# Kernel tuning notes

Hardware: AMD Instinct MI355X
Metric: run time of the kernel (lower is better)

The kernel has to match this reference:

```python
import jax, jax.numpy as jnp
import numpy as np

D_MODEL = 512
N_HEADS = 8
HEAD_DIM = D_MODEL // N_HEADS
D_FF = 2048
RADIUS = 1                      # manhattan_radius
MAX_LEVEL = 2                   # layer_max_level
WINDOWS = (512, 64, 16)         # window_size_per_level


def _layer_norm(x, g, b, eps=1e-5):
    mu = jnp.mean(x, axis=-1, keepdims=True)
    var = jnp.mean(jnp.square(x - mu), axis=-1, keepdims=True)
    return (x - mu) * jax.lax.rsqrt(var + eps) * g + b


def setup_inputs() -> dict:
    key = jax.random.key(0)
    ks = jax.random.split(key, 16)
    B, N = 2, 2048
    s = 0.02
    return {
        "x": jax.random.normal(ks[0], (B, N, D_MODEL), jnp.float32),
        "coords_pos": jax.random.randint(ks[1], (B, N, 2), 0, 64, jnp.int32),
        "coords_level": jax.random.randint(ks[2], (B, N), 0, 3, jnp.int32),
        "w_qkv": jax.random.normal(ks[3], (D_MODEL, 3 * D_MODEL), jnp.float32) * s,
        "b_qkv": jnp.zeros((3 * D_MODEL,), jnp.float32),
        "w_out": jax.random.normal(ks[4], (D_MODEL, D_MODEL), jnp.float32) * s,
        "b_out": jnp.zeros((D_MODEL,), jnp.float32),
        "w_ff1": jax.random.normal(ks[5], (D_MODEL, D_FF), jnp.float32) * s,
        "b_ff1": jnp.zeros((D_FF,), jnp.float32),
        "w_ff2": jax.random.normal(ks[6], (D_FF, D_MODEL), jnp.float32) * s,
        "b_ff2": jnp.zeros((D_MODEL,), jnp.float32),
        "ln1_g": jnp.ones((D_MODEL,), jnp.float32),
        "ln1_b": jnp.zeros((D_MODEL,), jnp.float32),
        "ln2_g": jnp.ones((D_MODEL,), jnp.float32),
        "ln2_b": jnp.zeros((D_MODEL,), jnp.float32),
    }


def _geometric_mask(coords_pos, coords_level):
    """[B,N,N] bool mask: same hierarchy level, Manhattan distance <= RADIUS,
    within the per-level sequence window, levels <= MAX_LEVEL; self always allowed."""
    B, N = coords_level.shape
    # Manhattan distance on grid coords  [B,N,N]
    dist = jnp.sum(jnp.abs(coords_pos[:, :, None, :] - coords_pos[:, None, :, :]), axis=-1)
    same_level = coords_level[:, :, None] == coords_level[:, None, :]
    lvl_ok = coords_level <= MAX_LEVEL                       # [B,N]
    lvl_pair = lvl_ok[:, :, None] & lvl_ok[:, None, :]
    win_tab = jnp.array(WINDOWS, jnp.int32)
    win_q = win_tab[jnp.clip(coords_level, 0, len(WINDOWS) - 1)]  # [B,N]
    idx = jnp.arange(N, dtype=jnp.int32)
    seq_dist = jnp.abs(idx[:, None] - idx[None, :])          # [N,N]
    in_window = seq_dist[None] < win_q[:, :, None]
    eye = jnp.eye(N, dtype=bool)[None]
    return (same_level & (dist <= RADIUS) & in_window & lvl_pair) | eye


def reference(x, coords_pos, coords_level, w_qkv, b_qkv, w_out, b_out,
              w_ff1, b_ff1, w_ff2, b_ff2, ln1_g, ln1_b, ln2_g, ln2_b):
    B, N, D = x.shape
    residual = x
    xn = _layer_norm(x, ln1_g, ln1_b)
    qkv = (xn @ w_qkv + b_qkv).reshape(B, N, 3, N_HEADS, HEAD_DIM)
    q, k, v = qkv[:, :, 0], qkv[:, :, 1], qkv[:, :, 2]        # [B,N,H,Dh]

    scale = 1.0 / np.sqrt(HEAD_DIM)
    scores = jnp.einsum("bihd,bjhd->bhij", q, k) * scale      # [B,H,N,N]
    mask = _geometric_mask(coords_pos, coords_level)          # [B,N,N]
    scores = jnp.where(mask[:, None], scores, jnp.float32(-1e9))
    probs = jax.nn.softmax(scores, axis=-1)
    attn = jnp.einsum("bhij,bjhd->bihd", probs, v).reshape(B, N, D)
    x = residual + (attn @ w_out + b_out)                     # dropout = identity (eval)

    residual = x
    xn = _layer_norm(x, ln2_g, ln2_b)
    h = jax.nn.gelu(xn @ w_ff1 + b_ff1, approximate=False)
    x = residual + (h @ w_ff2 + b_ff2)
    return x
```

## Files before the change

### kernel.cpp

```cpp
#include <hip/hip_runtime.h>
#include <hip/hip_bf16.h>

#define DMODEL 512
#define NHEADS 8
#define DFF 2048
#define NSEQ 2048
#define NROWS 4096

typedef __attribute__((ext_vector_type(8))) short   bf16x8;
typedef __attribute__((ext_vector_type(4))) float   f32x4;
typedef __attribute__((ext_vector_type(8))) unsigned short u16x8;

__device__ __forceinline__ unsigned short f2bf(float f) {
  union { float f; unsigned u; } v; v.f = f;
  unsigned r = v.u + 0x7fffu + ((v.u >> 16) & 1u);
  return (unsigned short)(r >> 16);
}
__device__ __forceinline__ float bf2f(unsigned short u) {
  union { unsigned u; float f; } v; v.u = (unsigned)u << 16;
  return v.f;
}

#define GLL16(src, dst) \
  __builtin_amdgcn_global_load_lds((__attribute__((address_space(1))) const void*)(src), \
                                   (__attribute__((address_space(3))) void*)(dst), 16, 0, 0)

__global__ __launch_bounds__(64)
void ln_kernel(const float* __restrict__ x, const float* __restrict__ g,
               const float* __restrict__ b, unsigned short* __restrict__ out) {
  const int row = blockIdx.x;
  const int lane = threadIdx.x;
  const float* xr = x + (size_t)row * DMODEL + lane * 8;
  const float4 v0 = *(const float4*)(xr);
  const float4 v1 = *(const float4*)(xr + 4);
  float s  = v0.x + v0.y + v0.z + v0.w + v1.x + v1.y + v1.z + v1.w;
  float s2 = v0.x*v0.x + v0.y*v0.y + v0.z*v0.z + v0.w*v0.w
           + v1.x*v1.x + v1.y*v1.y + v1.z*v1.z + v1.w*v1.w;
  #pragma unroll
  for (int m = 1; m < 64; m <<= 1) {
    s  += __shfl_xor(s,  m);
    s2 += __shfl_xor(s2, m);
  }
  const float mu  = s * (1.0f / DMODEL);
  const float var = s2 * (1.0f / DMODEL) - mu * mu;
  const float rs  = rsqrtf(var + 1e-5f);
  const float4 g0 = *(const float4*)(g + lane * 8);
  const float4 g1 = *(const float4*)(g + lane * 8 + 4);
  const float4 b0 = *(const float4*)(b + lane * 8);
  const float4 b1 = *(const float4*)(b + lane * 8 + 4);
  u16x8 o;
  o[0] = f2bf((v0.x - mu) * rs * g0.x + b0.x);
  o[1] = f2bf((v0.y - mu) * rs * g0.y + b0.y);
  o[2] = f2bf((v0.z - mu) * rs * g0.z + b0.z);
  o[3] = f2bf((v0.w - mu) * rs * g0.w + b0.w);
  o[4] = f2bf((v1.x - mu) * rs * g1.x + b1.x);
  o[5] = f2bf((v1.y - mu) * rs * g1.y + b1.y);
  o[6] = f2bf((v1.z - mu) * rs * g1.z + b1.z);
  o[7] = f2bf((v1.w - mu) * rs * g1.w + b1.w);
  *(u16x8*)(out + (size_t)row * DMODEL + lane * 8) = o;
}

__global__ __launch_bounds__(256)
void wt_all(const float* __restrict__ w0, unsigned short* __restrict__ t0,
            const float* __restrict__ w1, unsigned short* __restrict__ t1,
            const float* __restrict__ w2, unsigned short* __restrict__ t2,
            const float* __restrict__ w3, unsigned short* __restrict__ t3) {
  __shared__ unsigned short t[32][33];
  int bid = blockIdx.x;
  const float* w; unsigned short* wT; int K, N;
  if (bid < 768)       { w = w0; wT = t0; K = 512;  N = 1536; }
  else if (bid < 1024) { bid -= 768;  w = w1; wT = t1; K = 512;  N = 512; }
  else if (bid < 2048) { bid -= 1024; w = w2; wT = t2; K = 512;  N = 2048; }
  else                 { bid -= 2048; w = w3; wT = t3; K = 2048; N = 512; }
  const int ntx = N >> 5;
  const int n0 = (bid % ntx) * 32, k0 = (bid / ntx) * 32;
  const int tx = threadIdx.x, ty = threadIdx.y;
  #pragma unroll
  for (int i = 0; i < 4; ++i)
    t[ty + i * 8][tx] = f2bf(w[(size_t)(k0 + ty + i * 8) * N + n0 + tx]);
  __syncthreads();
  #pragma unroll
  for (int i = 0; i < 4; ++i)
    wT[(size_t)(n0 + ty + i * 8) * K + k0 + tx] = t[tx][ty + i * 8];
}

template<int MODE, int BM>
__global__ __launch_bounds__(256)
void gemm_bf16(const unsigned short* __restrict__ A,
               const unsigned short* __restrict__ Bt,
               const float* __restrict__ bias, const float* __restrict__ res,
               void* __restrict__ Cout, int M, int N, int LDA, int KL) {
  constexpr int MR = BM / 32;
  constexpr int PS = BM / 32 + 2;
  __shared__ unsigned short As[3][BM * 64];
  __shared__ unsigned short Bs[3][64 * 64];

  const int tid = threadIdx.x;
  const int w = tid >> 6, l = tid & 63;
  const int gx = N >> 6;
  const int nxy = gx * (M / BM);
  int lin = blockIdx.x;
  lin = (lin & 7) * (nxy >> 3) + (lin >> 3);
  const int bn = (lin % gx) << 6;
  const int bm = (lin / gx) * BM;
  const int wr = (w >> 1) * (BM >> 1);
  const int wc = (w & 1) * 32;
  const int lr = l & 15, kg = l >> 4;

  f32x4 acc[MR][2] = {};

  auto stage = [&](int buf, int k0) {
    #pragma unroll
    for (int i = 0; i < BM / 32; ++i) {
      const int g = i * 4 + w;
      const int c = g * 64 + l;
      const int row = c >> 3, kc = c & 7;
      GLL16(A + (size_t)(bm + row) * LDA + k0 + kc * 8, &As[buf][g * 512]);
    }
    #pragma unroll
    for (int i = 0; i < 2; ++i) {
      const int g = i * 4 + w;
      const int c = g * 64 + l;
      const int row = c >> 3, kc = c & 7;
      GLL16(Bt + (size_t)(bn + row) * LDA + k0 + kc * 8, &Bs[buf][g * 512]);
    }
  };

  const int nt = KL >> 6;
  stage(0, 0);
  stage(1, 64);
  for (int t = 0; t < nt; ++t) {
    if (t + 1 < nt) {
      asm volatile("s_waitcnt vmcnt(%0)" :: "n"(PS) : "memory");
    } else {
      asm volatile("s_waitcnt vmcnt(0)" ::: "memory");
    }
    __builtin_amdgcn_sched_barrier(0);
    __builtin_amdgcn_s_barrier();
    __builtin_amdgcn_sched_barrier(0);
    if (t + 2 < nt) stage((t + 2) % 3, (t + 2) << 6);
    const int cur = t % 3;
    #pragma unroll
    for (int ks = 0; ks < 2; ++ks) {
      const int cc = ks * 4 + kg;
      bf16x8 af[MR], bfv[2];
      #pragma unroll
      for (int mi = 0; mi < MR; ++mi)
        af[mi] = *(const bf16x8*)&As[cur][(wr + mi * 16 + lr) * 64 + cc * 8];
      #pragma unroll
      for (int ni = 0; ni < 2; ++ni)
        bfv[ni] = *(const bf16x8*)&Bs[cur][(wc + ni * 16 + lr) * 64 + cc * 8];
      __builtin_amdgcn_s_setprio(1);
      #pragma unroll
      for (int mi = 0; mi < MR; ++mi)
        #pragma unroll
        for (int ni = 0; ni < 2; ++ni)
          acc[mi][ni] = __builtin_amdgcn_mfma_f32_16x16x32_bf16(
              af[mi], bfv[ni], acc[mi][ni], 0, 0, 0);
      __builtin_amdgcn_s_setprio(0);
    }
  }

  float* Cf = (float*)Cout;
  unsigned short* Cb = (unsigned short*)Cout;
  #pragma unroll
  for (int mi = 0; mi < MR; ++mi) {
    #pragma unroll
    for (int ni = 0; ni < 2; ++ni) {
      const int gcol = bn + wc + ni * 16 + lr;
      const int grow0 = bm + wr + mi * 16 + kg * 4;
      const float bv = bias[gcol];
      #pragma unroll
      for (int reg = 0; reg < 4; ++reg) {
        const int grow = grow0 + reg;
        float t = acc[mi][ni][reg] + bv;
        if (MODE == 1) t += res[(size_t)grow * N + gcol];
        if (MODE == 2) t = 0.5f * t * (1.0f + erff(t * 0.70710678118654752f));
        if (MODE >= 2) Cb[(size_t)grow * N + gcol] = f2bf(t);
        else           Cf[(size_t)grow * N + gcol] = t;
      }
    }
  }
}

#define CAP 256
__global__ __launch_bounds__(64)
void attn_kernel(const unsigned short* __restrict__ qkv,
                 const int* __restrict__ pos, const int* __restrict__ lvl,
                 unsigned short* __restrict__ out) {
  const int r = blockIdx.x;
  const int i = r & (NSEQ - 1);
  const int base = r - i;
  const int lane = threadIdx.x;

  __shared__ int   s_idx[CAP];
  __shared__ int   s_cnt;
  __shared__ float s_sc[NHEADS][CAP];
  __shared__ float s_inv[NHEADS];

  if (lane == 0) s_cnt = 0;
  __syncthreads();

  const int li = lvl[r];
  const int2 pq = *(const int2*)(pos + 2 * r);
  const int win = (li == 0) ? 512 : (li == 1 ? 64 : 16);
  const int jlo = max(i - win + 1, 0);
  const int jhi = min(i + win - 1, NSEQ - 1);

  for (int j = jlo + lane; j <= jhi; j += 64) {
    const int rj = base + j;
    bool m = (j == i);
    if (!m) {
      const int lj = lvl[rj];
      const int2 pj = *(const int2*)(pos + 2 * rj);
      const int d = abs(pq.x - pj.x) + abs(pq.y - pj.y);
      m = (lj == li) && (d <= 1);
    }
    if (m) {
      const int p = atomicAdd(&s_cnt, 1);
      if (p < CAP) s_idx[p] = j;
    }
  }
  __syncthreads();
  const int cnt = min(s_cnt, CAP);

  const u16x8 qv = *(const u16x8*)(qkv + (size_t)r * 1536 + lane * 8);
  float qf[8];
  #pragma unroll
  for (int e = 0; e < 8; ++e) qf[e] = bf2f(qv[e]);

  for (int jj = 0; jj < cnt; ++jj) {
    const int rj = base + s_idx[jj];
    const u16x8 kv = *(const u16x8*)(qkv + (size_t)rj * 1536 + 512 + lane * 8);
    float p = 0.0f;
    #pragma unroll
    for (int e = 0; e < 8; ++e) p = fmaf(qf[e], bf2f(kv[e]), p);
    p += __shfl_xor(p, 1);
    p += __shfl_xor(p, 2);
    p += __shfl_xor(p, 4);
    if ((lane & 7) == 0) s_sc[lane >> 3][jj] = p * 0.125f;
  }
  __syncthreads();

  if (lane < 8) {
    float mx = -1e30f;
    for (int jj = 0; jj < cnt; ++jj) mx = fmaxf(mx, s_sc[lane][jj]);
    float den = 0.0f;
    for (int jj = 0; jj < cnt; ++jj) {
      const float e = expf(s_sc[lane][jj] - mx);
      s_sc[lane][jj] = e;
      den += e;
    }
    s_inv[lane] = 1.0f / den;
  }
  __syncthreads();

  const int h = lane >> 3;
  float a[8] = {};
  for (int jj = 0; jj < cnt; ++jj) {
    const float pp = s_sc[h][jj];
    const u16x8 vv = *(const u16x8*)(qkv + (size_t)(base + s_idx[jj]) * 1536 + 1024 + lane * 8);
    #pragma unroll
    for (int e = 0; e < 8; ++e) a[e] = fmaf(pp, bf2f(vv[e]), a[e]);
  }
  const float inv = s_inv[h];
  u16x8 o;
  #pragma unroll
  for (int e = 0; e < 8; ++e) o[e] = f2bf(a[e] * inv);
  *(u16x8*)(out + (size_t)r * DMODEL + lane * 8) = o;
}

extern "C" void kernel_launch(void* const* d_in, const int* in_sizes, int n_in,
                              void* d_out, int out_size, void* d_ws, size_t ws_size,
                              hipStream_t stream) {
  const float* x            = (const float*)d_in[0];
  const int*   coords_pos   = (const int*)d_in[1];
  const int*   coords_level = (const int*)d_in[2];
  const float* w_qkv        = (const float*)d_in[3];
  const float* b_qkv        = (const float*)d_in[4];
  const float* w_out        = (const float*)d_in[5];
  const float* b_out        = (const float*)d_in[6];
  const float* w_ff1        = (const float*)d_in[7];
  const float* b_ff1        = (const float*)d_in[8];
  const float* w_ff2        = (const float*)d_in[9];
  const float* b_ff2        = (const float*)d_in[10];
  const float* ln1_g        = (const float*)d_in[11];
  const float* ln1_b        = (const float*)d_in[12];
  const float* ln2_g        = (const float*)d_in[13];
  const float* ln2_b        = (const float*)d_in[14];
  float* out = (float*)d_out;

  char* ws = (char*)d_ws;
  unsigned short* qkv_bf = (unsigned short*)(ws);
  unsigned short* h_bf   = (unsigned short*)(ws);
  float*          x1     = (float*)(ws + 16777216);
  unsigned short* xn_bf  = (unsigned short*)(ws + 25165824);
  unsigned short* at_bf  = (unsigned short*)(ws + 29360128);
  unsigned short* wqkvT  = (unsigned short*)(ws + 33554432);
  unsigned short* woutT  = (unsigned short*)(ws + 35127296);
  unsigned short* wff1T  = (unsigned short*)(ws + 35651584);
  unsigned short* wff2T  = (unsigned short*)(ws + 37748736);

  wt_all<<<3072, dim3(32, 8), 0, stream>>>(w_qkv, wqkvT, w_out, woutT,
                                           w_ff1, wff1T, w_ff2, wff2T);

  ln_kernel<<<NROWS, 64, 0, stream>>>(x, ln1_g, ln1_b, xn_bf);
  gemm_bf16<3, 128><<<(1536/64)*(NROWS/128), 256, 0, stream>>>(
      xn_bf, wqkvT, b_qkv, nullptr, qkv_bf, NROWS, 1536, DMODEL, DMODEL);
  attn_kernel<<<NROWS, 64, 0, stream>>>(qkv_bf, coords_pos, coords_level, at_bf);
  gemm_bf16<1, 64><<<(DMODEL/64)*(NROWS/64), 256, 0, stream>>>(
      at_bf, woutT, b_out, x, x1, NROWS, DMODEL, DMODEL, DMODEL);
  ln_kernel<<<NROWS, 64, 0, stream>>>(x1, ln2_g, ln2_b, xn_bf);
  gemm_bf16<2, 128><<<(DFF/64)*(NROWS/128), 256, 0, stream>>>(
      xn_bf, wff1T, b_ff1, nullptr, h_bf, NROWS, DFF, DMODEL, DMODEL);
  gemm_bf16<1, 64><<<(DMODEL/64)*(NROWS/64), 256, 0, stream>>>(
      h_bf, wff2T, b_ff2, x1, out, NROWS, DMODEL, DFF, DFF);
}
```

Measured before the change: 112.3 us.

## Fold LayerNorm into GEMM epilogues via gamma-scaled weights and row stats

Removes both standalone LayerNorm kernels. Gamma is folded into the transposed weights, and per-column correction vectors (W·beta + bias, W·gamma) are precomputed. The QKV and FF1 GEMMs then apply the mean and rsqrt correction in their epilogue on raw bf16 inputs. The out-projection GEMM writes x1 in bf16 and accumulates per-row sum and sum-of-squares with atomics for LN2. The weight transpose, LN1 stats, x cast and stats zeroing are merged into one prep kernel. This trades two launches and fp32 round trips for extra epilogue work and atomics, and it adds precision risk from the unnormalized bf16 inputs and from storing the residual x1 in bf16.

New measurement: 157.1 us. 1.4x slower.

```diff
diff --git a/kernel.cpp b/kernel.cpp
--- a/kernel.cpp
+++ b/kernel.cpp
@@ -25,71 +25,100 @@
   __builtin_amdgcn_global_load_lds((__attribute__((address_space(1))) const void*)(src), \
                                    (__attribute__((address_space(3))) void*)(dst), 16, 0, 0)
 
-__global__ __launch_bounds__(64)
-void ln_kernel(const float* __restrict__ x, const float* __restrict__ g,
-               const float* __restrict__ b, unsigned short* __restrict__ out) {
-  const int row = blockIdx.x;
-  const int lane = threadIdx.x;
-  const float* xr = x + (size_t)row * DMODEL + lane * 8;
-  const float4 v0 = *(const float4*)(xr);
-  const float4 v1 = *(const float4*)(xr + 4);
-  float s  = v0.x + v0.y + v0.z + v0.w + v1.x + v1.y + v1.z + v1.w;
-  float s2 = v0.x*v0.x + v0.y*v0.y + v0.z*v0.z + v0.w*v0.w
-           + v1.x*v1.x + v1.y*v1.y + v1.z*v1.z + v1.w*v1.w;
-  #pragma unroll
-  for (int m = 1; m < 64; m <<= 1) {
-    s  += __shfl_xor(s,  m);
-    s2 += __shfl_xor(s2, m);
-  }
-  const float mu  = s * (1.0f / DMODEL);
-  const float var = s2 * (1.0f / DMODEL) - mu * mu;
-  const float rs  = rsqrtf(var + 1e-5f);
-  const float4 g0 = *(const float4*)(g + lane * 8);
-  const float4 g1 = *(const float4*)(g + lane * 8 + 4);
-  const float4 b0 = *(const float4*)(b + lane * 8);
-  const float4 b1 = *(const float4*)(b + lane * 8 + 4);
-  u16x8 o;
-  o[0] = f2bf((v0.x - mu) * rs * g0.x + b0.x);
-  o[1] = f2bf((v0.y - mu) * rs * g0.y + b0.y);
-  o[2] = f2bf((v0.z - mu) * rs * g0.z + b0.z);
-  o[3] = f2bf((v0.w - mu) * rs * g0.w + b0.w);
-  o[4] = f2bf((v1.x - mu) * rs * g1.x + b1.x);
-  o[5] = f2bf((v1.y - mu) * rs * g1.y + b1.y);
-  o[6] = f2bf((v1.z - mu) * rs * g1.z + b1.z);
-  o[7] = f2bf((v1.w - mu) * rs * g1.w + b1.w);
-  *(u16x8*)(out + (size_t)row * DMODEL + lane * 8) = o;
-}
-
 __global__ __launch_bounds__(256)
-void wt_all(const float* __restrict__ w0, unsigned short* __restrict__ t0,
-            const float* __restrict__ w1, unsigned short* __restrict__ t1,
-            const float* __restrict__ w2, unsigned short* __restrict__ t2,
-            const float* __restrict__ w3, unsigned short* __restrict__ t3) {
-  __shared__ unsigned short t[32][33];
+void prep(const float* __restrict__ w_qkv, const float* __restrict__ w_out,
+          const float* __restrict__ w_ff1, const float* __restrict__ w_ff2,
+          const float* __restrict__ ln1_g, const float* __restrict__ ln1_b,
+          const float* __restrict__ ln2_g, const float* __restrict__ ln2_b,
+          const float* __restrict__ b_qkv, const float* __restrict__ b_ff1,
+          const float* __restrict__ x,
+          unsigned short* __restrict__ wqkvT, unsigned short* __restrict__ woutT,
+          unsigned short* __restrict__ wff1T, unsigned short* __restrict__ wff2T,
+          float* __restrict__ vq, float* __restrict__ uq,
+          float* __restrict__ vf, float* __restrict__ uf,
+          unsigned short* __restrict__ x_bf, float2* __restrict__ stats1,
+          float* __restrict__ stats2) {
   int bid = blockIdx.x;
-  const float* w; unsigned short* wT; int K, N;
-  if (bid < 768)       { w = w0; wT = t0; K = 512;  N = 1536; }
-  else if (bid < 1024) { bid -= 768;  w = w1; wT = t1; K = 512;  N = 512; }
-  else if (bid < 2048) { bid -= 1024; w = w2; wT = t2; K = 512;  N = 2048; }
-  else                 { bid -= 2048; w = w3; wT = t3; K = 2048; N = 512; }
-  const int ntx = N >> 5;
-  const int n0 = (bid % ntx) * 32, k0 = (bid / ntx) * 32;
-  const int tx = threadIdx.x, ty = threadIdx.y;
-  #pragma unroll
-  for (int i = 0; i < 4; ++i)
-    t[ty + i * 8][tx] = f2bf(w[(size_t)(k0 + ty + i * 8) * N + n0 + tx]);
-  __syncthreads();
-  #pragma unroll
-  for (int i = 0; i < 4; ++i)
-    wT[(size_t)(n0 + ty + i * 8) * K + k0 + tx] = t[tx][ty + i * 8];
+  const int tid = threadIdx.x;
+  if (bid < 3072) {
+    __shared__ unsigned short t[32][33];
+    const float* w; unsigned short* wT; const float* g; int K, N;
+    if (bid < 768)       { w = w_qkv; wT = wqkvT; g = ln1_g; K = 512;  N = 1536; }
+    else if (bid < 1024) { bid -= 768;  w = w_out; wT = woutT; g = nullptr; K = 512;  N = 512; }
+    else if (bid < 2048) { bid -= 1024; w = w_ff1; wT = wff1T; g = ln2_g; K = 512;  N = 2048; }
+    else                 { bid -= 2048; w = w_ff2; wT = wff2T; g = nullptr; K = 2048; N = 512; }
+    const int ntx = N >> 5;
+    const int n0 = (bid % ntx) * 32, k0 = (bid / ntx) * 32;
+    const int tx = tid & 31, ty = tid >> 5;
+    #pragma unroll
+    for (int i = 0; i < 4; ++i) {
+      const int k = k0 + ty + i * 8;
+      const float s = g ? g[k] : 1.0f;
+      t[ty + i * 8][tx] = f2bf(s * w[(size_t)k * N + n0 + tx]);
+    }
+    __syncthreads();
+    #pragma unroll
+    for (int i = 0; i < 4; ++i)
+      wT[(size_t)(n0 + ty + i * 8) * K + k0 + tx] = t[tx][ty + i * 8];
+  } else if (bid < 3086) {
+    int n = (bid - 3072) * 256 + tid;
+    if (n < 1536) {
+      float u = 0.0f, v = 0.0f;
+      #pragma unroll 4
+      for (int k = 0; k < 512; ++k) {
+        const float wv = w_qkv[(size_t)k * 1536 + n];
+        u = fmaf(ln1_b[k], wv, u);
+        v = fmaf(ln1_g[k], wv, v);
+      }
+      vq[n] = v; uq[n] = u + b_qkv[n];
+    } else {
+      n -= 1536;
+      float u = 0.0f, v = 0.0f;
+      #pragma unroll 4
+      for (int k = 0; k < 512; ++k) {
+        const float wv = w_ff1[(size_t)k * 2048 + n];
+        u = fmaf(ln2_b[k], wv, u);
+        v = fmaf(ln2_g[k], wv, v);
+      }
+      vf[n] = v; uf[n] = u + b_ff1[n];
+    }
+  } else if (bid < 4110) {
+    const int row = (bid - 3086) * 4 + (tid >> 6);
+    const int lane = tid & 63;
+    const float* xr = x + (size_t)row * DMODEL + lane * 8;
+    const float4 v0 = *(const float4*)(xr);
+    const float4 v1 = *(const float4*)(xr + 4);
+    float s  = v0.x + v0.y + v0.z + v0.w + v1.x + v1.y + v1.z + v1.w;
+    float s2 = v0.x*v0.x + v0.y*v0.y + v0.z*v0.z + v0.w*v0.w
+             + v1.x*v1.x + v1.y*v1.y + v1.z*v1.z + v1.w*v1.w;
+    #pragma unroll
+    for (int m = 1; m < 64; m <<= 1) {
+      s  += __shfl_xor(s,  m);
+      s2 += __shfl_xor(s2, m);
+    }
+    const float mu  = s * (1.0f / DMODEL);
+    const float var = s2 * (1.0f / DMODEL) - mu * mu;
+    const float rs  = rsqrtf(var + 1e-5f);
+    if (lane == 0) stats1[row] = make_float2(mu, rs);
+    u16x8 o;
+    o[0] = f2bf(v0.x); o[1] = f2bf(v0.y); o[2] = f2bf(v0.z); o[3] = f2bf(v0.w);
+    o[4] = f2bf(v1.x); o[5] = f2bf(v1.y); o[6] = f2bf(v1.z); o[7] = f2bf(v1.w);
+    *(u16x8*)(x_bf + (size_t)row * DMODEL + lane * 8) = o;
+  } else {
+    const int idx = (bid - 4110) * 256 + tid;
+    if (idx < 2 * NROWS) stats2[idx] = 0.0f;
+  }
 }
 
 template<int MODE, int BM>
 __global__ __launch_bounds__(256)
 void gemm_bf16(const unsigned short* __restrict__ A,
                const unsigned short* __restrict__ Bt,
-               const float* __restrict__ bias, const float* __restrict__ res,
-               void* __restrict__ Cout, int M, int N, int LDA, int KL) {
+               const float* __restrict__ bias,
+               const float* __restrict__ v, const float* __restrict__ u,
+               const float* __restrict__ resf, const unsigned short* __restrict__ resb,
+               float* __restrict__ stats, void* __restrict__ Cout,
+               int M, int N, int LDA, int KL) {
   constexpr int MR = BM / 32;
   constexpr int PS = BM / 32 + 2;
   __shared__ unsigned short As[3][BM * 64];
@@ -166,18 +195,44 @@
   #pragma unroll
   for (int mi = 0; mi < MR; ++mi) {
     #pragma unroll
-    for (int ni = 0; ni < 2; ++ni) {
-      const int gcol = bn + wc + ni * 16 + lr;
-      const int grow0 = bm + wr + mi * 16 + kg * 4;
-      const float bv = bias[gcol];
+    for (int reg = 0; reg < 4; ++reg) {
+      const int grow = bm + wr + mi * 16 + kg * 4 + reg;
+      float mu = 0.0f, rs = 0.0f;
+      if (MODE == 4) {
+        const float2 st = ((const float2*)stats)[grow];
+        mu = st.x; rs = st.y;
+      }
+      if (MODE == 6) {
+        const float2 st = ((const float2*)stats)[grow];
+        mu = st.x * (1.0f / DMODEL);
+        rs = rsqrtf(st.y * (1.0f / DMODEL) - mu * mu + 1e-5f);
+      }
+      float vals[2];
       #pragma unroll
-      for (int reg = 0; reg < 4; ++reg) {
-        const int grow = grow0 + reg;
-        float t = acc[mi][ni][reg] + bv;
-        if (MODE == 1) t += res[(size_t)grow * N + gcol];
-        if (MODE == 2) t = 0.5f * t * (1.0f + erff(t * 0.70710678118654752f));
-        if (MODE >= 2) Cb[(size_t)grow * N + gcol] = f2bf(t);
-        else           Cf[(size_t)grow * N + gcol] = t;
+      for (int ni = 0; ni < 2; ++ni) {
+        const int gcol = bn + wc + ni * 16 + lr;
+        float t = acc[mi][ni][reg];
+        if (MODE == 4 || MODE == 6) t = rs * (t - mu * v[gcol]) + u[gcol];
+        else                        t += bias[gcol];
+        if (MODE == 5) t += resf[(size_t)grow * N + gcol];
+        if (MODE == 7) t += bf2f(resb[(size_t)grow * N + gcol]);
+        if (MODE == 6) t = 0.5f * t * (1.0f + erff(t * 0.70710678118654752f));
+        if (MODE == 7) Cf[(size_t)grow * N + gcol] = t;
+        else           Cb[(size_t)grow * N + gcol] = f2bf(t);
+        vals[ni] = t;
+      }
+      if (MODE == 5) {
+        float rsum = vals[0] + vals[1];
+        float rsq  = vals[0] * vals[0] + vals[1] * vals[1];
+        #pragma unroll
+        for (int m = 1; m < 16; m <<= 1) {
+          rsum += __shfl_xor(rsum, m);
+          rsq  += __shfl_xor(rsq,  m);
+        }
+        if (lr == 0) {
+          atomicAdd(&stats[2 * grow],     rsum);
+          atomicAdd(&stats[2 * grow + 1], rsq);
+        }
       }
     }
   }
@@ -293,26 +348,40 @@
   char* ws = (char*)d_ws;
   unsigned short* qkv_bf = (unsigned short*)(ws);
   unsigned short* h_bf   = (unsigned short*)(ws);
-  float*          x1     = (float*)(ws + 16777216);
-  unsigned short* xn_bf  = (unsigned short*)(ws + 25165824);
-  unsigned short* at_bf  = (unsigned short*)(ws + 29360128);
-  unsigned short* wqkvT  = (unsigned short*)(ws + 33554432);
-  unsigned short* woutT  = (unsigned short*)(ws + 35127296);
-  unsigned short* wff1T  = (unsigned short*)(ws + 35651584);
-  unsigned short* wff2T  = (unsigned short*)(ws + 37748736);
-
-  wt_all<<<3072, dim3(32, 8), 0, stream>>>(w_qkv, wqkvT, w_out, woutT,
-                                           w_ff1, wff1T, w_ff2, wff2T);
-
-  ln_kernel<<<NROWS, 64, 0, stream>>>(x, ln1_g, ln1_b, xn_bf);
-  gemm_bf16<3, 128><<<(1536/64)*(NROWS/128), 256, 0, stream>>>(
-      xn_bf, wqkvT, b_qkv, nullptr, qkv_bf, NROWS, 1536, DMODEL, DMODEL);
+  unsigned short* x_bf   = (unsigned short*)(ws + 16777216);
+  unsigned short* at_bf  = (unsigned short*)(ws + 20971520);
+  unsigned short* x1_bf  = (unsigned short*)(ws + 25165824);
+  unsigned short* wqkvT  = (unsigned short*)(ws + 29360128);
+  unsigned short* woutT  = (unsigned short*)(ws + 30932992);
+  unsigned short* wff1T  = (unsigned short*)(ws + 31457280);
+  unsigned short* wff2T  = (unsigned short*)(ws + 33554432);
+  float*          vq     = (float*)(ws + 35651584);
+  float*          uq     = (float*)(ws + 35657728);
+  float*          vf     = (float*)(ws + 35663872);
+  float*          uf     = (float*)(ws + 35672064);
+  float2*         stats1 = (float2*)(ws + 35680256);
+  float*          stats2 = (float*)(ws + 35713024);
+
+  prep<<<4142, 256, 0, stream>>>(w_qkv, w_out, w_ff1, w_ff2,
+                                 ln1_g, ln1_b, ln2_g, ln2_b, b_qkv, b_ff1, x,
+                                 wqkvT, woutT, wff1T, wff2T,
+                                 vq, uq, vf, uf, x_bf, stats1, stats2);
+
+  gemm_bf16<4, 128><<<(1536/64)*(NROWS/128), 256, 0, stream>>>(
+      x_bf, wqkvT, nullptr, vq, uq, nullptr, nullptr, (float*)stats1,
+      qkv_bf, NROWS, 1536, DMODEL, DMODEL);
+
   attn_kernel<<<NROWS, 64, 0, stream>>>(qkv_bf, coords_pos, coords_level, at_bf);
-  gemm_bf16<1, 64><<<(DMODEL/64)*(NROWS/64), 256, 0, stream>>>(
-      at_bf, woutT, b_out, x, x1, NROWS, DMODEL, DMODEL, DMODEL);
-  ln_kernel<<<NROWS, 64, 0, stream>>>(x1, ln2_g, ln2_b, xn_bf);
-  gemm_bf16<2, 128><<<(DFF/64)*(NROWS/128), 256, 0, stream>>>(
-      xn_bf, wff1T, b_ff1, nullptr, h_bf, NROWS, DFF, DMODEL, DMODEL);
-  gemm_bf16<1, 64><<<(DMODEL/64)*(NROWS/64), 256, 0, stream>>>(
-      h_bf, wff2T, b_ff2, x1, out, NROWS, DMODEL, DFF, DFF);
-}
+
+  gemm_bf16<5, 64><<<(DMODEL/64)*(NROWS/64), 256, 0, stream>>>(
+      at_bf, woutT, b_out, nullptr, nullptr, x, nullptr, stats2,
+      x1_bf, NROWS, DMODEL, DMODEL, DMODEL);
+
+  gemm_bf16<6, 128><<<(DFF/64)*(NROWS/128), 256, 0, stream>>>(
+      x1_bf, wff1T, nullptr, vf, uf, nullptr, nullptr, stats2,
+      h_bf, NROWS, DFF, DMODEL, DMODEL);
+
+  gemm_bf16<7, 64><<<(DMODEL/64)*(NROWS/64), 256, 0, stream>>>(
+      h_bf, wff2T, b_ff2, nullptr, nullptr, nullptr, x1_bf, nullptr,
+      out, NROWS, DMODEL, DFF, DFF);
+}
```
